# Optimization experiments

Measured on AMD Instinct MI355X. Metric: run time of the kernel, lower is better.

The kernel has to match this reference:

```python
import jax, jax.numpy as jnp
import numpy as np

S, H, W_GRID, F, B = 256, 256, 256, 6, 4096


def setup_inputs() -> dict:
    key = jax.random.key(0)
    k1, k2, k3, k4 = jax.random.split(key, 4)
    feats = jax.random.normal(k1, (B, 2, F), dtype=jnp.float32)
    # coordinate channels 6..9 hold integer grid indices stored as floats
    coords = jax.random.randint(k2, (B, 2, 4), 0, H).astype(jnp.float32)
    phi = jnp.concatenate([feats, coords], axis=-1)            # [B, 2, 10]
    w_lin = jax.random.normal(k3, (1, F), dtype=jnp.float32) * 0.1
    succ_feats = jax.random.normal(k4, (S, H, W_GRID, F), dtype=jnp.float32)
    return {"phi": phi, "w_lin": w_lin, "succ_feats": succ_feats}


def _get_vals(succ_feats, w_lin, xs, ys):
    # xs, ys: [B, 2] int32 grid coordinates
    sel = succ_feats[:, xs, ys]                 # [S, B, 2, F] gather
    sel = jnp.transpose(sel, (1, 0, 2, 3))      # [B, S, 2, F]
    vs = jnp.einsum('bstf,of->bsto', sel, w_lin)  # [B, S, 2, 1]
    p = jax.nn.softmax(vs, axis=1)              # softmax over S states
    return jnp.sum(p * vs, axis=1)[..., 0]      # [B, 2]


def reference(phi, w_lin, succ_feats):
    pr = jnp.einsum('btf,of->bto', phi[:, :, 0:F], w_lin)[..., 0]  # [B, 2]
    ss_x = phi[:, :, 6].astype(jnp.int32)
    ss_y = phi[:, :, 7].astype(jnp.int32)
    es_x = phi[:, :, 8].astype(jnp.int32)
    es_y = phi[:, :, 9].astype(jnp.int32)
    # get_vals runs under torch.no_grad() in the original -> stop_gradient
    v_ss = jax.lax.stop_gradient(_get_vals(succ_feats, w_lin, ss_x, ss_y))
    v_es = jax.lax.stop_gradient(_get_vals(succ_feats, w_lin, es_x, es_y))
    left_der = pr[:, 0:1] + (v_es[:, 0:1] - v_ss[:, 0:1])   # [B, 1]
    right_der = pr[:, 1:2] + (v_es[:, 1:2] - v_ss[:, 1:2])  # [B, 1]
    left_pred = jax.nn.sigmoid(left_der - right_der)
    right_pred = jax.nn.sigmoid(right_der - left_der)
    return jnp.stack([left_pred, right_pred], axis=1)        # [B, 2, 1]
```

## Files before the change

### kernel.cpp

```cpp
#include <hip/hip_runtime.h>
#include <math.h>

#define S_DIM 256
#define H_DIM 256
#define W_DIM 256
#define F_DIM 6
#define B_DIM 4096

__global__ __launch_bounds__(1024) void build_vtable(const float* __restrict__ succ,
                                                     const float* __restrict__ w_lin,
                                                     float* __restrict__ V) {
    __shared__ float sm[8][256];
    __shared__ float sl[8][256];
    __shared__ float sn[8][256];

    const int x   = blockIdx.x;
    const int tid = threadIdx.x;
    const int p   = tid & 127;
    const int c   = tid >> 7;
    const int y0  = p * 2;

    const float w0 = w_lin[0], w1 = w_lin[1], w2 = w_lin[2],
                w3 = w_lin[3], w4 = w_lin[4], w5 = w_lin[5];

    float m0 = -INFINITY, l0 = 0.f, n0 = 0.f;
    float m1 = -INFINITY, l1 = 0.f, n1 = 0.f;

    size_t elem = ((size_t)((c * 32) * H_DIM + x) * W_DIM + y0) * F_DIM;
    const float4* ptr = (const float4*)(succ + elem);
    const size_t stride4 = (size_t)H_DIM * W_DIM * F_DIM / 4;

    #pragma unroll 4
    for (int i = 0; i < 32; ++i) {
        float4 a = ptr[0];
        float4 b = ptr[1];
        float4 d = ptr[2];
        ptr += stride4;

        float v0 = a.x*w0 + a.y*w1 + a.z*w2 + a.w*w3 + b.x*w4 + b.y*w5;
        float v1 = b.z*w0 + b.w*w1 + d.x*w2 + d.y*w3 + d.z*w4 + d.w*w5;

        float nm0 = fmaxf(m0, v0);
        float sc0 = __expf(m0 - nm0);
        float e0  = __expf(v0 - nm0);
        l0 = l0 * sc0 + e0;
        n0 = n0 * sc0 + e0 * v0;
        m0 = nm0;

        float nm1 = fmaxf(m1, v1);
        float sc1 = __expf(m1 - nm1);
        float e1  = __expf(v1 - nm1);
        l1 = l1 * sc1 + e1;
        n1 = n1 * sc1 + e1 * v1;
        m1 = nm1;
    }

    sm[c][y0] = m0; sm[c][y0+1] = m1;
    sl[c][y0] = l0; sl[c][y0+1] = l1;
    sn[c][y0] = n0; sn[c][y0+1] = n1;
    __syncthreads();

    if (tid < 256) {
        float M = sm[0][tid];
        #pragma unroll
        for (int cc = 1; cc < 8; ++cc) M = fmaxf(M, sm[cc][tid]);
        float L = 0.f, N = 0.f;
        #pragma unroll
        for (int cc = 0; cc < 8; ++cc) {
            float sc = __expf(sm[cc][tid] - M);
            L += sl[cc][tid] * sc;
            N += sn[cc][tid] * sc;
        }
        V[x * 256 + tid] = N / L;
    }
}

__global__ void eval_queries(const float* __restrict__ phi,
                             const float* __restrict__ w_lin,
                             const float* __restrict__ V,
                             float* __restrict__ out) {
    const int b = blockIdx.x * blockDim.x + threadIdx.x;
    if (b >= B_DIM) return;

    const float w0 = w_lin[0], w1 = w_lin[1], w2 = w_lin[2],
                w3 = w_lin[3], w4 = w_lin[4], w5 = w_lin[5];

    const float* p = phi + (size_t)b * 20;
    float der[2];
    #pragma unroll
    for (int t = 0; t < 2; ++t) {
        const float* q = p + t * 10;
        float pr = q[0]*w0 + q[1]*w1 + q[2]*w2 + q[3]*w3 + q[4]*w4 + q[5]*w5;
        int ssx = (int)q[6];
        int ssy = (int)q[7];
        int esx = (int)q[8];
        int esy = (int)q[9];
        float v_ss = V[ssx * 256 + ssy];
        float v_es = V[esx * 256 + esy];
        der[t] = pr + (v_es - v_ss);
    }
    float d = der[0] - der[1];
    out[b * 2 + 0] = 1.f / (1.f + __expf(-d));
    out[b * 2 + 1] = 1.f / (1.f + __expf(d));
}

extern "C" void kernel_launch(void* const* d_in, const int* in_sizes, int n_in,
                              void* d_out, int out_size, void* d_ws, size_t ws_size,
                              hipStream_t stream) {
    const float* phi   = (const float*)d_in[0];
    const float* w_lin = (const float*)d_in[1];
    const float* succ  = (const float*)d_in[2];
    float* out = (float*)d_out;
    float* V   = (float*)d_ws;

    build_vtable<<<256, 1024, 0, stream>>>(succ, w_lin, V);
    eval_queries<<<(B_DIM + 255) / 256, 256, 0, stream>>>(phi, w_lin, V, out);
}
```

Measured before the change: 519.2 us.

## Compute value table only for grid cells referenced by queries

Measured after the change: 516.3 us. Within noise of the previous version (-0.6%).

```diff
diff --git a/kernel.cpp b/kernel.cpp
--- a/kernel.cpp
+++ b/kernel.cpp
@@ -6,61 +6,96 @@
 #define W_DIM 256
 #define F_DIM 6
 #define B_DIM 4096
+#define SLICE ((size_t)H_DIM * W_DIM * F_DIM)
 
-__global__ __launch_bounds__(1024) void build_vtable(const float* __restrict__ succ,
-                                                     const float* __restrict__ w_lin,
-                                                     float* __restrict__ V) {
+
+__global__ __launch_bounds__(1024) void build_mask(const float* __restrict__ phi,
+                                                   unsigned int* __restrict__ mask) {
+    __shared__ unsigned int lmask[2048];
+    const int tid = threadIdx.x;
+    lmask[tid] = 0u;
+    lmask[tid + 1024] = 0u;
+    __syncthreads();
+    for (int r = tid; r < B_DIM * 2; r += 1024) {
+        const float* q = phi + (size_t)r * 10;
+        float2 a = *(const float2*)(q + 6);
+        float2 b = *(const float2*)(q + 8);
+        int c0 = ((int)a.x) * 256 + (int)a.y;
+        int c1 = ((int)b.x) * 256 + (int)b.y;
+        atomicOr(&lmask[c0 >> 5], 1u << (c0 & 31));
+        atomicOr(&lmask[c1 >> 5], 1u << (c1 & 31));
+    }
+    __syncthreads();
+    mask[tid] = lmask[tid];
+    mask[tid + 1024] = lmask[tid + 1024];
+}
+
+__global__ __launch_bounds__(1024) void build_vtable_sparse(const float* __restrict__ succ,
+                                                            const float* __restrict__ w_lin,
+                                                            const unsigned int* __restrict__ mask,
+                                                            float* __restrict__ V) {
+    __shared__ unsigned int rowmask[8];
+    __shared__ int cellIdx[256];
+    __shared__ int nCellsSh;
     __shared__ float sm[8][256];
     __shared__ float sl[8][256];
     __shared__ float sn[8][256];
 
     const int x   = blockIdx.x;
     const int tid = threadIdx.x;
-    const int p   = tid & 127;
-    const int c   = tid >> 7;
-    const int y0  = p * 2;
+
+    if (tid < 8) rowmask[tid] = mask[x * 8 + tid];
+    __syncthreads();
+
+    if (tid < 256) {
+        const int w = tid >> 5, bit = tid & 31;
+        const unsigned int mw = rowmask[w];
+        int rank = 0;
+        #pragma unroll
+        for (int k = 0; k < 8; ++k)
+            if (k < w) rank += __popc(rowmask[k]);
+        rank += __popc(mw & (bit ? ((1u << bit) - 1u) : 0u));
+        if ((mw >> bit) & 1u) cellIdx[rank] = tid;
+        if (tid == 0) {
+            int n = 0;
+            #pragma unroll
+            for (int k = 0; k < 8; ++k) n += __popc(rowmask[k]);
+            nCellsSh = n;
+        }
+    }
+    __syncthreads();
+    const int nCells = nCellsSh;
 
     const float w0 = w_lin[0], w1 = w_lin[1], w2 = w_lin[2],
                 w3 = w_lin[3], w4 = w_lin[4], w5 = w_lin[5];
 
-    float m0 = -INFINITY, l0 = 0.f, n0 = 0.f;
-    float m1 = -INFINITY, l1 = 0.f, n1 = 0.f;
+    const int c     = tid >> 7;
+    const int slot0 = tid & 127;
 
-    size_t elem = ((size_t)((c * 32) * H_DIM + x) * W_DIM + y0) * F_DIM;
-    const float4* ptr = (const float4*)(succ + elem);
-    const size_t stride4 = (size_t)H_DIM * W_DIM * F_DIM / 4;
-
-    #pragma unroll 4
-    for (int i = 0; i < 32; ++i) {
-        float4 a = ptr[0];
-        float4 b = ptr[1];
-        float4 d = ptr[2];
-        ptr += stride4;
-
-        float v0 = a.x*w0 + a.y*w1 + a.z*w2 + a.w*w3 + b.x*w4 + b.y*w5;
-        float v1 = b.z*w0 + b.w*w1 + d.x*w2 + d.y*w3 + d.z*w4 + d.w*w5;
-
-        float nm0 = fmaxf(m0, v0);
-        float sc0 = __expf(m0 - nm0);
-        float e0  = __expf(v0 - nm0);
-        l0 = l0 * sc0 + e0;
-        n0 = n0 * sc0 + e0 * v0;
-        m0 = nm0;
-
-        float nm1 = fmaxf(m1, v1);
-        float sc1 = __expf(m1 - nm1);
-        float e1  = __expf(v1 - nm1);
-        l1 = l1 * sc1 + e1;
-        n1 = n1 * sc1 + e1 * v1;
-        m1 = nm1;
+    for (int slot = slot0; slot < nCells; slot += 128) {
+        const int y = cellIdx[slot];
+        const float* p = succ + (size_t)(c * 32) * SLICE
+                              + (size_t)(x * W_DIM + y) * F_DIM;
+        float m = -INFINITY, l = 0.f, n = 0.f;
+        #pragma unroll 8
+        for (int i = 0; i < 32; ++i) {
+            float2 a = ((const float2*)p)[0];
+            float2 b = ((const float2*)p)[1];
+            float2 d = ((const float2*)p)[2];
+            p += SLICE;
+            float v = a.x*w0 + a.y*w1 + b.x*w2 + b.y*w3 + d.x*w4 + d.y*w5;
+            float nm = fmaxf(m, v);
+            float sc = __expf(m - nm);
+            float e  = __expf(v - nm);
+            l = l * sc + e;
+            n = n * sc + e * v;
+            m = nm;
+        }
+        sm[c][slot] = m; sl[c][slot] = l; sn[c][slot] = n;
     }
-
-    sm[c][y0] = m0; sm[c][y0+1] = m1;
-    sl[c][y0] = l0; sl[c][y0+1] = l1;
-    sn[c][y0] = n0; sn[c][y0+1] = n1;
     __syncthreads();
 
-    if (tid < 256) {
+    if (tid < 256 && tid < nCells) {
         float M = sm[0][tid];
         #pragma unroll
         for (int cc = 1; cc < 8; ++cc) M = fmaxf(M, sm[cc][tid]);
@@ -71,7 +106,7 @@
             L += sl[cc][tid] * sc;
             N += sn[cc][tid] * sc;
         }
-        V[x * 256 + tid] = N / L;
+        V[x * 256 + cellIdx[tid]] = N / L;
     }
 }
 
@@ -111,8 +146,11 @@
     const float* w_lin = (const float*)d_in[1];
     const float* succ  = (const float*)d_in[2];
     float* out = (float*)d_out;
-    float* V   = (float*)d_ws;
 
-    build_vtable<<<256, 1024, 0, stream>>>(succ, w_lin, V);
+    float* V = (float*)d_ws;
+    unsigned int* mask = (unsigned int*)(V + 65536);
+
+    build_mask<<<1, 1024, 0, stream>>>(phi, mask);
+    build_vtable_sparse<<<256, 1024, 0, stream>>>(succ, w_lin, mask, V);
     eval_queries<<<(B_DIM + 255) / 256, 256, 0, stream>>>(phi, w_lin, V, out);
 }
```
